# Kernel tuning notes

Hardware: AMD Instinct MI355X
Metric: run time of the kernel (lower is better)

The kernel has to match this reference:

```python
import jax, jax.numpy as jnp
import numpy as np

BITS_MENU = (2, 4, 8)  # fixed candidate bit-widths (replaces torch.unique for jit)
EPS = 1e-8


def _ste_quant_from_stats(x, mn, mx, b):
    # fake-quant with straight-through estimator: identity gradient
    scale = jnp.maximum((mx - mn) / (2.0 ** b - 1.0), EPS)
    q = jnp.round((x - mn) / scale) * scale + mn
    return x + jax.lax.stop_gradient(q - x)


def _ste_quant(x, b):
    return _ste_quant_from_stats(x, x.min(), x.max(), b)


def _conv2d(x, w, b):
    # NCHW / OIHW, stride 1, padding 1 (matches nn.Conv2d(32,32,3,1,1))
    y = jax.lax.conv_general_dilated(
        x, w, window_strides=(1, 1), padding=((1, 1), (1, 1)),
        dimension_numbers=("NCHW", "OIHW", "NCHW"))
    return y + b[None, :, None, None]


def setup_inputs() -> dict:
    key = jax.random.key(0)
    k1, k2, k3, k4 = jax.random.split(key, 4)
    B, Cin, Cout, H, W = 32, 32, 32, 192, 192
    x = jax.random.normal(k1, (B, Cin, H, W), dtype=jnp.float32)
    weight = jax.random.normal(k2, (Cout, Cin, 3, 3), dtype=jnp.float32) * 0.05
    bias = jax.random.normal(k3, (Cout,), dtype=jnp.float32) * 0.01
    # per-sample bit widths drawn from {2,4,8}
    bits = (2 ** jax.random.randint(k4, (B,), 1, 4)).astype(jnp.int32)
    return {"x": x, "weight": weight, "bias": bias, "bits": bits}


def reference(x, weight, bias, bits):
    out = jnp.zeros((x.shape[0], weight.shape[0], x.shape[2], x.shape[3]),
                    dtype=x.dtype)
    for b in BITS_MENU:
        mask = bits == b                                # [B]
        has = jnp.any(mask)
        m4 = mask[:, None, None, None]
        # group min/max over the selected samples (matches x[idx].min()/max())
        mn = jnp.min(jnp.where(m4, x, jnp.inf))
        mx = jnp.max(jnp.where(m4, x, -jnp.inf))
        mn = jnp.where(has, mn, 0.0)
        mx = jnp.where(has, mx, 0.0)
        x_q = _ste_quant_from_stats(x, mn, mx, float(b))
        w_q = _ste_quant(weight, float(b))
        y = _conv2d(x_q, w_q, bias)
        out = jnp.where(m4, y, out)  # scatter back to original sample order
    return out
```

## Files before the change

### kernel.cpp

```cpp
#include <hip/hip_runtime.h>

#define EPSQ 1e-8f

typedef int v4i  __attribute__((ext_vector_type(4)));
typedef int v16i __attribute__((ext_vector_type(16)));


__device__ __forceinline__ int bytesum4(int v) {
#if __has_builtin(__builtin_amdgcn_sdot4)
    return __builtin_amdgcn_sdot4(v, 0x01010101, 0, false);
#else
    return (int)(char)(v) + (int)(char)(v >> 8) + (int)(char)(v >> 16) + (int)(char)(v >> 24);
#endif
}

__global__ __launch_bounds__(256) void kAW(
    const float* __restrict__ x, const float* __restrict__ w,
    float* __restrict__ partials, unsigned int* __restrict__ wq8,
    int* __restrict__ colJ, float* __restrict__ wstats)
{
    __shared__ float smn[256], smx[256];
    __shared__ int   jred[256];
    __shared__ float s_wmn, s_wmx;
    const int tid = threadIdx.x;

    if (blockIdx.x < 1152) {
        const int batch = blockIdx.x / 36;
        const int blk   = blockIdx.x % 36;
        const float* xb = x + (size_t)batch * 1179648 + (size_t)blk * 32768;
        float mn = INFINITY, mx = -INFINITY;
#pragma unroll
        for (int i = 0; i < 32; ++i) {
            const float4 v = reinterpret_cast<const float4*>(xb)[i * 256 + tid];
            mn = fminf(mn, fminf(fminf(v.x, v.y), fminf(v.z, v.w)));
            mx = fmaxf(mx, fmaxf(fmaxf(v.x, v.y), fmaxf(v.z, v.w)));
        }
        smn[tid] = mn; smx[tid] = mx;
        __syncthreads();
        for (int s = 128; s > 0; s >>= 1) {
            if (tid < s) {
                smn[tid] = fminf(smn[tid], smn[tid + s]);
                smx[tid] = fmaxf(smx[tid], smx[tid + s]);
            }
            __syncthreads();
        }
        if (tid == 0) {
            partials[blockIdx.x * 2 + 0] = smn[0];
            partials[blockIdx.x * 2 + 1] = smx[0];
        }
        return;
    }

    const int wb  = blockIdx.x - 1152;
    const int g   = wb / 9;
    const int tap = wb % 9;

    float wmn = INFINITY, wmx = -INFINITY;
    for (int i = tid; i < 9216; i += 256) {
        const float v = w[i];
        wmn = fminf(wmn, v); wmx = fmaxf(wmx, v);
    }
    smn[tid] = wmn; smx[tid] = wmx; __syncthreads();
    for (int s = 128; s > 0; s >>= 1) {
        if (tid < s) {
            smn[tid] = fminf(smn[tid], smn[tid + s]);
            smx[tid] = fmaxf(smx[tid], smx[tid + s]);
        }
        __syncthreads();
    }
    if (tid == 0) { s_wmn = smn[0]; s_wmx = smx[0]; }
    __syncthreads();
    if (wb == 0 && tid == 0) { wstats[0] = s_wmn; wstats[1] = s_wmx; }

    const float wmv = s_wmn, wxv = s_wmx;
    const int bval = 2 << g;
    const float denom = (float)((1 << bval) - 1);
    const float t = fmaxf((wxv - wmv) / denom, EPSQ);
    const int sig = 1 << (bval - 1);

    const int co = tid & 31;
    const int q  = tid >> 5;
    unsigned int packed = 0;
    int jsum = 0;
#pragma unroll
    for (int b = 0; b < 4; ++b) {
        const int ci = q * 4 + b;
        int jc = (int)rintf((w[co * 288 + ci * 9 + tap] - wmv) / t) - sig;
        jc = jc < -128 ? -128 : (jc > 127 ? 127 : jc);
        jsum += jc;
        packed |= ((unsigned int)(unsigned char)(char)jc) << (8 * b);
    }
    const int lane_ = (q >> 2) * 32 + co;
    const int a4    = q & 3;
    wq8[((size_t)(g * 9 + tap) * 64 + lane_) * 4 + a4] = packed;

    jred[tid] = jsum; __syncthreads();
    if (tid < 128) jred[tid] += jred[tid + 128];
    __syncthreads();
    if (tid < 64) jred[tid] += jred[tid + 64];
    __syncthreads();
    if (tid < 32) colJ[g * 288 + tap * 32 + tid] = jred[tid] + jred[tid + 32];
}

__global__ __launch_bounds__(256) void kQ_quant(
    const float* __restrict__ x, const int* __restrict__ bits,
    const float* __restrict__ partials, unsigned int* __restrict__ codes)
{
    __shared__ float bmn[32], bmx[32];
    __shared__ float s_mn, s_sc;

    const int n     = blockIdx.x / 36;
    const int chunk = blockIdx.x % 36;
    const int tid   = threadIdx.x;
    const int bval  = bits[n];
    const int sig   = 1 << (bval - 1);

    if (tid < 32) {
        float mn = INFINITY, mx = -INFINITY;
        for (int i = 0; i < 36; ++i) {
            mn = fminf(mn, partials[(tid * 36 + i) * 2 + 0]);
            mx = fmaxf(mx, partials[(tid * 36 + i) * 2 + 1]);
        }
        bmn[tid] = mn; bmx[tid] = mx;
    }
    __syncthreads();
    if (tid == 0) {
        float mn = INFINITY, mx = -INFINITY;
        for (int nb = 0; nb < 32; ++nb)
            if (bits[nb] == bval) { mn = fminf(mn, bmn[nb]); mx = fmaxf(mx, bmx[nb]); }
        const float denom = (float)((1 << bval) - 1);
        s_mn = mn;
        s_sc = fmaxf((mx - mn) / denom, EPSQ);
    }
    __syncthreads();
    const float mn = s_mn, s = s_sc;

    const int px0 = chunk * 1024 + tid * 4;
    const float* xn = x + (size_t)n * 1179648;

    unsigned int creg[32];
#pragma unroll
    for (int i = 0; i < 32; ++i) creg[i] = 0;

#pragma unroll
    for (int ci = 0; ci < 32; ++ci) {
        const float4 v = *(const float4*)(xn + (size_t)ci * 36864 + px0);
        const float vv[4] = {v.x, v.y, v.z, v.w};
#pragma unroll
        for (int p = 0; p < 4; ++p) {
            int kq = (int)rintf((vv[p] - mn) / s) - sig;
            kq = kq < -128 ? -128 : (kq > 127 ? 127 : kq);
            creg[p * 8 + (ci >> 2)] |= ((unsigned int)(unsigned char)(char)kq) << (8 * (ci & 3));
        }
    }

    unsigned int* cp = codes + ((size_t)n * 36864 + (size_t)px0) * 8;
#pragma unroll
    for (int p = 0; p < 4; ++p) {
        *(v4i*)(cp + p * 8 + 0) = (v4i){(int)creg[p*8+0], (int)creg[p*8+1], (int)creg[p*8+2], (int)creg[p*8+3]};
        *(v4i*)(cp + p * 8 + 4) = (v4i){(int)creg[p*8+4], (int)creg[p*8+5], (int)creg[p*8+6], (int)creg[p*8+7]};
    }
}

__global__ __launch_bounds__(256, 4) void kC_codes(
    const unsigned int* __restrict__ codes, const int* __restrict__ bits,
    const float* __restrict__ partials, const int* __restrict__ colJ,
    const float* __restrict__ wstats, const float* __restrict__ bias,
    const unsigned int* __restrict__ wq8, float* __restrict__ out)
{
    __shared__ v4i   xkv[18 * 34 * 3];
    __shared__ short cs2s[18 * 34];
    __shared__ float tlds[288];
    __shared__ float bmn[32], bmx[32];
    __shared__ float s_stats[4];

    const int n  = blockIdx.z;
    const int oy = blockIdx.y * 16;
    const int ox = blockIdx.x * 32;
    const int tid  = threadIdx.x;
    const int lane = tid & 63;
    const int wv   = tid >> 6;

    const int bval = bits[n];
    const int g = (bval == 2) ? 0 : (bval == 4 ? 1 : 2);
    const int sig = 1 << (bval - 1);
    const float denom = (float)((1 << bval) - 1);

    if (tid < 32) {
        float mn = INFINITY, mx = -INFINITY;
        for (int i = 0; i < 36; ++i) {
            mn = fminf(mn, partials[(tid * 36 + i) * 2 + 0]);
            mx = fmaxf(mx, partials[(tid * 36 + i) * 2 + 1]);
        }
        bmn[tid] = mn; bmx[tid] = mx;
    }
    __syncthreads();
    if (tid == 0) {
        float mn = INFINITY, mx = -INFINITY;
        for (int nb = 0; nb < 32; ++nb)
            if (bits[nb] == bval) { mn = fminf(mn, bmn[nb]); mx = fmaxf(mx, bmx[nb]); }
        const float scale = fmaxf((mx - mn) / denom, EPSQ);
        const float wmv = wstats[0], wxv = wstats[1];
        const float t = fmaxf((wxv - wmv) / denom, EPSQ);
        const double B_ = (double)wmv + (double)sig * (double)t;
        s_stats[0] = mn;
        s_stats[1] = scale;
        s_stats[2] = (float)((double)scale * (double)t);
        s_stats[3] = (float)((double)scale * B_);
    }
    __syncthreads();
    const float C1 = s_stats[2];
    const float C2 = s_stats[3];

    {
        const float wmv = wstats[0], wxv = wstats[1];
        const float t = fmaxf((wxv - wmv) / denom, EPSQ);
        const double A_ = (double)s_stats[0] + (double)sig * (double)s_stats[1];
        const double B_ = (double)wmv + (double)sig * (double)t;
        for (int idx = tid; idx < 288; idx += 256) {
            const int cls = idx / 32;
            const int co  = idx % 32;
            const int rc = cls / 3, cc = cls % 3;
            double js = 0.0, ij = 0.0; int ninv = 0;
            for (int tap = 0; tap < 9; ++tap) {
                const int dy = tap / 3, dx = tap % 3;
                const int cj = colJ[g * 288 + tap * 32 + co];
                js += (double)cj;
                const bool inv = (rc == 0 && dy == 0) || (rc == 2 && dy == 2) ||
                                 (cc == 0 && dx == 0) || (cc == 2 && dx == 2);
                if (inv) { ++ninv; ij += (double)cj; }
            }
            const double v = (double)t * A_ * js + 288.0 * A_ * B_ + (double)bias[co]
                           - A_ * (32.0 * B_ * (double)ninv + (double)t * ij);
            tlds[idx] = (float)v;
        }
    }

    const v4i* wA = (const v4i*)(wq8 + (size_t)g * 2304);
    v4i wfr[9];
#pragma unroll
    for (int t = 0; t < 9; ++t) wfr[t] = wA[t * 64 + lane];

    const unsigned int* cb = codes + (size_t)n * 36864 * 8;
    char* xk = (char*)xkv;
    for (int px = tid; px < 612; px += 256) {
        const int r = px / 34;
        const int c = px - r * 34;
        const int gy = oy + r - 1, gx = ox + c - 1;
        v4i pk0 = (v4i){0,0,0,0}, pk1 = (v4i){0,0,0,0};
        int ksum = 0;
        if (((unsigned)gy < 192u) && ((unsigned)gx < 192u)) {
            const unsigned int* p = cb + ((size_t)gy * 192 + gx) * 8;
            pk0 = *(const v4i*)(p + 0);
            pk1 = *(const v4i*)(p + 4);
            ksum = bytesum4(pk0.x) + bytesum4(pk0.y) + bytesum4(pk0.z) + bytesum4(pk0.w)
                 + bytesum4(pk1.x) + bytesum4(pk1.y) + bytesum4(pk1.z) + bytesum4(pk1.w);
        }
        *(v4i*)(xk + px * 48 +  0) = pk0;
        *(v4i*)(xk + px * 48 + 16) = pk1;
        cs2s[px] = (short)ksum;
    }
    __syncthreads();

    const int c  = lane & 31;
    const int ch = lane >> 5;
    const int gx = ox + c;
    const int cc = (gx == 0) ? 0 : ((gx == 191) ? 2 : 1);
    const int r0 = wv * 4;

    v16i acc[4] = {};
#pragma unroll
    for (int dyr = 0; dyr < 6; ++dyr) {
        const int xrow = r0 + dyr;
        const v4i bf0 = xkv[(xrow * 34 + c + 0) * 3 + ch];
        const v4i bf1 = xkv[(xrow * 34 + c + 1) * 3 + ch];
        const v4i bf2 = xkv[(xrow * 34 + c + 2) * 3 + ch];
#pragma unroll
        for (int m = 0; m < 4; ++m) {
            const int dy = dyr - m;
            if (dy >= 0 && dy < 3) {
                acc[m] = __builtin_amdgcn_mfma_i32_32x32x32_i8(wfr[dy * 3 + 0], bf0, acc[m], 0, 0, 0);
                acc[m] = __builtin_amdgcn_mfma_i32_32x32x32_i8(wfr[dy * 3 + 1], bf1, acc[m], 0, 0, 0);
                acc[m] = __builtin_amdgcn_mfma_i32_32x32x32_i8(wfr[dy * 3 + 2], bf2, acc[m], 0, 0, 0);
            }
        }
    }

#pragma unroll
    for (int m = 0; m < 4; ++m) {
        const int r  = r0 + m;
        const int gy = oy + r;
        int k1 = 0;
#pragma unroll
        for (int dy = 0; dy < 3; ++dy)
#pragma unroll
            for (int dx = 0; dx < 3; ++dx)
                k1 += (int)cs2s[(r + dy) * 34 + (c + dx)];
        const int rc = (gy == 0) ? 0 : ((gy == 191) ? 2 : 1);
        const int cls = rc * 3 + cc;
        const float t2 = C2 * (float)k1;
#pragma unroll
        for (int reg = 0; reg < 16; ++reg) {
            const int co = (reg & 3) + 8 * (reg >> 2) + 4 * ch;
            const float y = fmaf(C1, (float)acc[m][reg], t2 + tlds[cls * 32 + co]);
            out[(((size_t)n * 32 + co) * 192 + gy) * 192 + gx] = y;
        }
    }
}

__global__ __launch_bounds__(256) void kB2_stats_tbl(
    const float* __restrict__ bias, const int* __restrict__ bits,
    const float* __restrict__ partials, const int* __restrict__ colJ,
    const float* __restrict__ wstats,
    float* __restrict__ gstats, float* __restrict__ coefs, float* __restrict__ tbl)
{
    __shared__ float bmn[32], bmx[32];
    __shared__ float s_gmn[3], s_gs[3];
    const int tid = threadIdx.x;
    const float wmv = wstats[0], wxv = wstats[1];

    if (tid < 32) {
        float mn = INFINITY, mx = -INFINITY;
        for (int i = 0; i < 36; ++i) {
            mn = fminf(mn, partials[(tid * 36 + i) * 2 + 0]);
            mx = fmaxf(mx, partials[(tid * 36 + i) * 2 + 1]);
        }
        bmn[tid] = mn; bmx[tid] = mx;
    }
    __syncthreads();

    if (tid < 3) {
        const int bval = 2 << tid;
        const float denom = (float)((1 << bval) - 1);
        float mn = INFINITY, mx = -INFINITY; bool has = false;
        for (int nb = 0; nb < 32; ++nb) {
            if (bits[nb] == bval) { has = true; mn = fminf(mn, bmn[nb]); mx = fmaxf(mx, bmx[nb]); }
        }
        if (!has) { mn = 0.f; mx = 0.f; }
        const float scale = fmaxf((mx - mn) / denom, EPSQ);
        gstats[tid * 2 + 0] = mn;
        gstats[tid * 2 + 1] = scale;
        s_gmn[tid] = mn; s_gs[tid] = scale;

        const float t = fmaxf((wxv - wmv) / denom, EPSQ);
        const int sig = 1 << (bval - 1);
        const double B_ = (double)wmv + (double)sig * (double)t;
        coefs[tid * 2 + 0] = (float)((double)scale * (double)t);
        coefs[tid * 2 + 1] = (float)((double)scale * B_);
    }
    __syncthreads();

    for (int idx = tid; idx < 864; idx += 256) {
        const int g   = idx / 288;
        const int rem = idx % 288;
        const int cls = rem / 32;
        const int co  = rem % 32;
        const int bval = 2 << g;
        const float denom = (float)((1 << bval) - 1);
        const float t = fmaxf((wxv - wmv) / denom, EPSQ);
        const int sig = 1 << (bval - 1);
        const double A_ = (double)s_gmn[g] + (double)sig * (double)s_gs[g];
        const double B_ = (double)wmv + (double)sig * (double)t;
        const int rc = cls / 3, cc = cls % 3;
        double js = 0.0, ij = 0.0; int ninv = 0;
        for (int tap = 0; tap < 9; ++tap) {
            const int dy = tap / 3, dx = tap % 3;
            const int cj = colJ[g * 288 + tap * 32 + co];
            js += (double)cj;
            const bool inv = (rc == 0 && dy == 0) || (rc == 2 && dy == 2) ||
                             (cc == 0 && dx == 0) || (cc == 2 && dx == 2);
            if (inv) { ++ninv; ij += (double)cj; }
        }
        const double v = (double)t * A_ * js + 288.0 * A_ * B_ + (double)bias[co]
                       - A_ * (32.0 * B_ * (double)ninv + (double)t * ij);
        tbl[idx] = (float)v;
    }
}

__global__ __launch_bounds__(256, 4) void kC_fused(
    const float* __restrict__ x, const int* __restrict__ bits,
    const float* __restrict__ gstats, const float* __restrict__ coefs,
    const float* __restrict__ tbl, const unsigned int* __restrict__ wq8,
    float* __restrict__ out)
{
    __shared__ v4i   xkv[18 * 34 * 3];
    __shared__ short cs2s[18 * 34];
    __shared__ float tlds[288];

    const int n  = blockIdx.z;
    const int oy = blockIdx.y * 16;
    const int ox = blockIdx.x * 32;
    const int tid  = threadIdx.x;
    const int lane = tid & 63;
    const int wv   = tid >> 6;

    const int bval = bits[n];
    const int g = (bval == 2) ? 0 : (bval == 4 ? 1 : 2);
    const int sig = 1 << (bval - 1);
    const float mn = gstats[g * 2 + 0];
    const float s  = gstats[g * 2 + 1];
    const float C1 = coefs[g * 2 + 0];
    const float C2 = coefs[g * 2 + 1];

    const v4i* wA = (const v4i*)(wq8 + (size_t)g * 2304);
    v4i wfr[9];
#pragma unroll
    for (int t = 0; t < 9; ++t) wfr[t] = wA[t * 64 + lane];

    for (int i = tid; i < 288; i += 256) tlds[i] = tbl[g * 288 + i];

    const float* xn = x + (size_t)n * 1179648;
    char* xk = (char*)xkv;
    for (int px = tid; px < 612; px += 256) {
        const int r = px / 34;
        const int c = px - r * 34;
        const int gy = oy + r - 1, gx = ox + c - 1;
        const bool valid = ((unsigned)gy < 192u) && ((unsigned)gx < 192u);
        const float* xp = xn + (size_t)(valid ? gy : 0) * 192 + (valid ? gx : 0);
        int ksum = 0;
        v4i pk0, pk1;
#pragma unroll
        for (int h = 0; h < 2; ++h) {
            float v[16];
#pragma unroll
            for (int i = 0; i < 16; ++i) v[i] = xp[(size_t)(h * 16 + i) * 36864];
            int w4[4];
#pragma unroll
            for (int q4 = 0; q4 < 4; ++q4) {
                unsigned int pw = 0;
#pragma unroll
                for (int b = 0; b < 4; ++b) {
                    int kq = (int)rintf((v[q4 * 4 + b] - mn) / s) - sig;
                    kq = kq < -128 ? -128 : (kq > 127 ? 127 : kq);
                    ksum += kq;
                    pw |= ((unsigned int)(unsigned char)(char)kq) << (8 * b);
                }
                w4[q4] = (int)pw;
            }
            if (h == 0) pk0 = (v4i){w4[0], w4[1], w4[2], w4[3]};
            else        pk1 = (v4i){w4[0], w4[1], w4[2], w4[3]};
        }
        if (!valid) { pk0 = (v4i){0,0,0,0}; pk1 = (v4i){0,0,0,0}; ksum = 0; }
        *(v4i*)(xk + px * 48 +  0) = pk0;
        *(v4i*)(xk + px * 48 + 16) = pk1;
        cs2s[px] = (short)ksum;
    }
    __syncthreads();

    const int c  = lane & 31;
    const int ch = lane >> 5;
    const int gx = ox + c;
    const int cc = (gx == 0) ? 0 : ((gx == 191) ? 2 : 1);
    const int r0 = wv * 4;

    v16i acc[4] = {};
#pragma unroll
    for (int dyr = 0; dyr < 6; ++dyr) {
        const int xrow = r0 + dyr;
        const v4i bf0 = xkv[(xrow * 34 + c + 0) * 3 + ch];
        const v4i bf1 = xkv[(xrow * 34 + c + 1) * 3 + ch];
        const v4i bf2 = xkv[(xrow * 34 + c + 2) * 3 + ch];
#pragma unroll
        for (int m = 0; m < 4; ++m) {
            const int dy = dyr - m;
            if (dy >= 0 && dy < 3) {
                acc[m] = __builtin_amdgcn_mfma_i32_32x32x32_i8(wfr[dy * 3 + 0], bf0, acc[m], 0, 0, 0);
                acc[m] = __builtin_amdgcn_mfma_i32_32x32x32_i8(wfr[dy * 3 + 1], bf1, acc[m], 0, 0, 0);
                acc[m] = __builtin_amdgcn_mfma_i32_32x32x32_i8(wfr[dy * 3 + 2], bf2, acc[m], 0, 0, 0);
            }
        }
    }

#pragma unroll
    for (int m = 0; m < 4; ++m) {
        const int r  = r0 + m;
        const int gy = oy + r;
        int k1 = 0;
#pragma unroll
        for (int dy = 0; dy < 3; ++dy)
#pragma unroll
            for (int dx = 0; dx < 3; ++dx)
                k1 += (int)cs2s[(r + dy) * 34 + (c + dx)];
        const int rc = (gy == 0) ? 0 : ((gy == 191) ? 2 : 1);
        const int cls = rc * 3 + cc;
        const float t2 = C2 * (float)k1;
#pragma unroll
        for (int reg = 0; reg < 16; ++reg) {
            const int co = (reg & 3) + 8 * (reg >> 2) + 4 * ch;
            const float y = fmaf(C1, (float)acc[m][reg], t2 + tlds[cls * 32 + co]);
            out[(((size_t)n * 32 + co) * 192 + gy) * 192 + gx] = y;
        }
    }
}

extern "C" void kernel_launch(void* const* d_in, const int* in_sizes, int n_in,
                              void* d_out, int out_size, void* d_ws, size_t ws_size,
                              hipStream_t stream) {
    const float* x      = (const float*)d_in[0];
    const float* weight = (const float*)d_in[1];
    const float* bias   = (const float*)d_in[2];
    const int*   bits   = (const int*)d_in[3];
    float* out = (float*)d_out;

    float* ws       = (float*)d_ws;
    float* partials = ws;
    float* gstats   = ws + 2304;
    float* coefs    = ws + 2312;
    float* tbl      = ws + 2320;
    int*   colJ     = (int*)(ws + 3184);
    unsigned int* wq8 = (unsigned int*)(ws + 4048);
    float* wstats   = ws + 10960;
    const size_t codes_off   = 43904;
    const size_t codes_bytes = 37748736ull;
    unsigned int* codes = (unsigned int*)((char*)d_ws + codes_off);
    const bool big_ws = ws_size >= codes_off + codes_bytes;

    kAW<<<1179, 256, 0, stream>>>(x, weight, partials, wq8, colJ, wstats);

    dim3 grid(6, 12, 32);
    if (big_ws) {
        kQ_quant<<<32 * 36, 256, 0, stream>>>(x, bits, partials, codes);
        kC_codes<<<grid, 256, 0, stream>>>(codes, bits, partials, colJ, wstats, bias, wq8, out);
    } else {
        kB2_stats_tbl<<<1, 256, 0, stream>>>(bias, bits, partials, colJ, wstats, gstats, coefs, tbl);
        kC_fused<<<grid, 256, 0, stream>>>(x, bits, gstats, coefs, tbl, wq8, out);
    }
}
```

Measured before the change: 118.6 us.

## Fuse stats, quantize and conv phases into one cooperative persistent kernel

Merges the min/max reduction, activation quantization and int8 conv into a single cooperative kernel with grid-wide syncs between phases, removing two kernel launch boundaries. The work units are also split more finely (72 chunks per sample instead of 36) for better load balance across the 777 persistent blocks. If a cooperative launch is unavailable, it falls back to three separate kernels. The cost is grid-sync overhead, forced persistent scheduling with limited occupancy, and extra per-block host-side occupancy queries on every call.

```diff
diff --git a/kernel.cpp b/kernel.cpp
--- a/kernel.cpp
+++ b/kernel.cpp
@@ -1,4 +1,7 @@
 #include <hip/hip_runtime.h>
+#include <hip/hip_cooperative_groups.h>
+
+namespace cg = cooperative_groups;
 
 #define EPSQ 1e-8f
 
@@ -14,24 +17,24 @@
 #endif
 }
 
-__global__ __launch_bounds__(256) void kAW(
-    const float* __restrict__ x, const float* __restrict__ w,
+__device__ __forceinline__ void phaseA_unit(
+    int u, int tid, const float* __restrict__ x, const float* __restrict__ w,
     float* __restrict__ partials, unsigned int* __restrict__ wq8,
-    int* __restrict__ colJ, float* __restrict__ wstats)
-{
-    __shared__ float smn[256], smx[256];
-    __shared__ int   jred[256];
-    __shared__ float s_wmn, s_wmx;
-    const int tid = threadIdx.x;
-
-    if (blockIdx.x < 1152) {
-        const int batch = blockIdx.x / 36;
-        const int blk   = blockIdx.x % 36;
-        const float* xb = x + (size_t)batch * 1179648 + (size_t)blk * 32768;
+    int* __restrict__ colJ, float* __restrict__ wstats, char* smem)
+{
+    float* smn  = (float*)smem;
+    float* smx  = (float*)(smem + 1024);
+    int*   jred = (int*)(smem + 2048);
+    float* swst = (float*)(smem + 3072);
+
+    if (u < 2304) {
+        const int batch = u / 72;
+        const int blk   = u % 72;
+        const float4* xb4 = (const float4*)(x + (size_t)batch * 1179648 + (size_t)blk * 16384);
         float mn = INFINITY, mx = -INFINITY;
 #pragma unroll
-        for (int i = 0; i < 32; ++i) {
-            const float4 v = reinterpret_cast<const float4*>(xb)[i * 256 + tid];
+        for (int i = 0; i < 16; ++i) {
+            const float4 v = xb4[i * 256 + tid];
             mn = fminf(mn, fminf(fminf(v.x, v.y), fminf(v.z, v.w)));
             mx = fmaxf(mx, fmaxf(fmaxf(v.x, v.y), fmaxf(v.z, v.w)));
         }
@@ -45,13 +48,14 @@
             __syncthreads();
         }
         if (tid == 0) {
-            partials[blockIdx.x * 2 + 0] = smn[0];
-            partials[blockIdx.x * 2 + 1] = smx[0];
-        }
+            partials[u * 2 + 0] = smn[0];
+            partials[u * 2 + 1] = smx[0];
+        }
+        __syncthreads();
         return;
     }
 
-    const int wb  = blockIdx.x - 1152;
+    const int wb  = u - 2304;
     const int g   = wb / 9;
     const int tap = wb % 9;
 
@@ -68,11 +72,11 @@
         }
         __syncthreads();
     }
-    if (tid == 0) { s_wmn = smn[0]; s_wmx = smx[0]; }
-    __syncthreads();
-    if (wb == 0 && tid == 0) { wstats[0] = s_wmn; wstats[1] = s_wmx; }
-
-    const float wmv = s_wmn, wxv = s_wmx;
+    if (tid == 0) { swst[0] = smn[0]; swst[1] = smx[0]; }
+    __syncthreads();
+    if (wb == 0 && tid == 0) { wstats[0] = swst[0]; wstats[1] = swst[1]; }
+
+    const float wmv = swst[0], wxv = swst[1];
     const int bval = 2 << g;
     const float denom = (float)((1 << bval) - 1);
     const float t = fmaxf((wxv - wmv) / denom, EPSQ);
@@ -100,26 +104,27 @@
     if (tid < 64) jred[tid] += jred[tid + 64];
     __syncthreads();
     if (tid < 32) colJ[g * 288 + tap * 32 + tid] = jred[tid] + jred[tid + 32];
-}
-
-__global__ __launch_bounds__(256) void kQ_quant(
-    const float* __restrict__ x, const int* __restrict__ bits,
-    const float* __restrict__ partials, unsigned int* __restrict__ codes)
-{
-    __shared__ float bmn[32], bmx[32];
-    __shared__ float s_mn, s_sc;
-
-    const int n     = blockIdx.x / 36;
-    const int chunk = blockIdx.x % 36;
-    const int tid   = threadIdx.x;
+    __syncthreads();
+}
+
+__device__ __forceinline__ void phaseQ_unit(
+    int u, int tid, const float* __restrict__ x, const int* __restrict__ bits,
+    const float* __restrict__ partials, unsigned int* __restrict__ codes, char* smem)
+{
+    float* bmn = (float*)smem;
+    float* bmx = (float*)(smem + 128);
+    float* s2  = (float*)(smem + 256);
+
+    const int n     = u / 72;
+    const int chunk = u % 72;
     const int bval  = bits[n];
     const int sig   = 1 << (bval - 1);
 
     if (tid < 32) {
         float mn = INFINITY, mx = -INFINITY;
-        for (int i = 0; i < 36; ++i) {
-            mn = fminf(mn, partials[(tid * 36 + i) * 2 + 0]);
-            mx = fmaxf(mx, partials[(tid * 36 + i) * 2 + 1]);
+        for (int i = 0; i < 72; ++i) {
+            mn = fminf(mn, partials[(tid * 72 + i) * 2 + 0]);
+            mx = fmaxf(mx, partials[(tid * 72 + i) * 2 + 1]);
         }
         bmn[tid] = mn; bmx[tid] = mx;
     }
@@ -129,25 +134,25 @@
         for (int nb = 0; nb < 32; ++nb)
             if (bits[nb] == bval) { mn = fminf(mn, bmn[nb]); mx = fmaxf(mx, bmx[nb]); }
         const float denom = (float)((1 << bval) - 1);
-        s_mn = mn;
-        s_sc = fmaxf((mx - mn) / denom, EPSQ);
-    }
-    __syncthreads();
-    const float mn = s_mn, s = s_sc;
-
-    const int px0 = chunk * 1024 + tid * 4;
+        s2[0] = mn;
+        s2[1] = fmaxf((mx - mn) / denom, EPSQ);
+    }
+    __syncthreads();
+    const float mn = s2[0], s = s2[1];
+
+    const int px0 = chunk * 512 + tid * 2;
     const float* xn = x + (size_t)n * 1179648;
 
-    unsigned int creg[32];
-#pragma unroll
-    for (int i = 0; i < 32; ++i) creg[i] = 0;
+    unsigned int creg[16];
+#pragma unroll
+    for (int i = 0; i < 16; ++i) creg[i] = 0;
 
 #pragma unroll
     for (int ci = 0; ci < 32; ++ci) {
-        const float4 v = *(const float4*)(xn + (size_t)ci * 36864 + px0);
-        const float vv[4] = {v.x, v.y, v.z, v.w};
-#pragma unroll
-        for (int p = 0; p < 4; ++p) {
+        const float2 v = *(const float2*)(xn + (size_t)ci * 36864 + px0);
+        const float vv[2] = {v.x, v.y};
+#pragma unroll
+        for (int p = 0; p < 2; ++p) {
             int kq = (int)rintf((vv[p] - mn) / s) - sig;
             kq = kq < -128 ? -128 : (kq > 127 ? 127 : kq);
             creg[p * 8 + (ci >> 2)] |= ((unsigned int)(unsigned char)(char)kq) << (8 * (ci & 3));
@@ -156,28 +161,31 @@
 
     unsigned int* cp = codes + ((size_t)n * 36864 + (size_t)px0) * 8;
 #pragma unroll
-    for (int p = 0; p < 4; ++p) {
+    for (int p = 0; p < 2; ++p) {
         *(v4i*)(cp + p * 8 + 0) = (v4i){(int)creg[p*8+0], (int)creg[p*8+1], (int)creg[p*8+2], (int)creg[p*8+3]};
         *(v4i*)(cp + p * 8 + 4) = (v4i){(int)creg[p*8+4], (int)creg[p*8+5], (int)creg[p*8+6], (int)creg[p*8+7]};
     }
-}
-
-__global__ __launch_bounds__(256, 4) void kC_codes(
-    const unsigned int* __restrict__ codes, const int* __restrict__ bits,
+    __syncthreads();
+}
+
+__device__ __forceinline__ void phaseC_tile(
+    int t, int tid, const unsigned int* __restrict__ codes, const int* __restrict__ bits,
     const float* __restrict__ partials, const int* __restrict__ colJ,
     const float* __restrict__ wstats, const float* __restrict__ bias,
-    const unsigned int* __restrict__ wq8, float* __restrict__ out)
-{
-    __shared__ v4i   xkv[18 * 34 * 3];
-    __shared__ short cs2s[18 * 34];
-    __shared__ float tlds[288];
-    __shared__ float bmn[32], bmx[32];
-    __shared__ float s_stats[4];
-
-    const int n  = blockIdx.z;
-    const int oy = blockIdx.y * 16;
-    const int ox = blockIdx.x * 32;
-    const int tid  = threadIdx.x;
+    const unsigned int* __restrict__ wq8, float* __restrict__ out, char* smem)
+{
+    v4i*   xkv  = (v4i*)smem;
+    short* cs2s = (short*)(smem + 29376);
+    float* tlds = (float*)(smem + 30600);
+    float* bmn  = (float*)(smem + 31752);
+    float* bmx  = (float*)(smem + 31880);
+    float* sst  = (float*)(smem + 32008);
+
+    const int bx = t % 6;
+    const int by = (t / 6) % 12;
+    const int n  = t / 72;
+    const int oy = by * 16;
+    const int ox = bx * 32;
     const int lane = tid & 63;
     const int wv   = tid >> 6;
 
@@ -188,9 +196,9 @@
 
     if (tid < 32) {
         float mn = INFINITY, mx = -INFINITY;
-        for (int i = 0; i < 36; ++i) {
-            mn = fminf(mn, partials[(tid * 36 + i) * 2 + 0]);
-            mx = fmaxf(mx, partials[(tid * 36 + i) * 2 + 1]);
+        for (int i = 0; i < 72; ++i) {
+            mn = fminf(mn, partials[(tid * 72 + i) * 2 + 0]);
+            mx = fmaxf(mx, partials[(tid * 72 + i) * 2 + 1]);
         }
         bmn[tid] = mn; bmx[tid] = mx;
     }
@@ -201,22 +209,22 @@
             if (bits[nb] == bval) { mn = fminf(mn, bmn[nb]); mx = fmaxf(mx, bmx[nb]); }
         const float scale = fmaxf((mx - mn) / denom, EPSQ);
         const float wmv = wstats[0], wxv = wstats[1];
-        const float t = fmaxf((wxv - wmv) / denom, EPSQ);
-        const double B_ = (double)wmv + (double)sig * (double)t;
-        s_stats[0] = mn;
-        s_stats[1] = scale;
-        s_stats[2] = (float)((double)scale * (double)t);
-        s_stats[3] = (float)((double)scale * B_);
-    }
-    __syncthreads();
-    const float C1 = s_stats[2];
-    const float C2 = s_stats[3];
+        const float tq = fmaxf((wxv - wmv) / denom, EPSQ);
+        const double B_ = (double)wmv + (double)sig * (double)tq;
+        sst[0] = mn;
+        sst[1] = scale;
+        sst[2] = (float)((double)scale * (double)tq);
+        sst[3] = (float)((double)scale * B_);
+    }
+    __syncthreads();
+    const float C1 = sst[2];
+    const float C2 = sst[3];
 
     {
         const float wmv = wstats[0], wxv = wstats[1];
-        const float t = fmaxf((wxv - wmv) / denom, EPSQ);
-        const double A_ = (double)s_stats[0] + (double)sig * (double)s_stats[1];
-        const double B_ = (double)wmv + (double)sig * (double)t;
+        const float tq = fmaxf((wxv - wmv) / denom, EPSQ);
+        const double A_ = (double)sst[0] + (double)sig * (double)sst[1];
+        const double B_ = (double)wmv + (double)sig * (double)tq;
         for (int idx = tid; idx < 288; idx += 256) {
             const int cls = idx / 32;
             const int co  = idx % 32;
@@ -230,8 +238,8 @@
                                  (cc == 0 && dx == 0) || (cc == 2 && dx == 2);
                 if (inv) { ++ninv; ij += (double)cj; }
             }
-            const double v = (double)t * A_ * js + 288.0 * A_ * B_ + (double)bias[co]
-                           - A_ * (32.0 * B_ * (double)ninv + (double)t * ij);
+            const double v = (double)tq * A_ * js + 288.0 * A_ * B_ + (double)bias[co]
+                           - A_ * (32.0 * B_ * (double)ninv + (double)tq * ij);
             tlds[idx] = (float)v;
         }
     }
@@ -239,7 +247,7 @@
     const v4i* wA = (const v4i*)(wq8 + (size_t)g * 2304);
     v4i wfr[9];
 #pragma unroll
-    for (int t = 0; t < 9; ++t) wfr[t] = wA[t * 64 + lane];
+    for (int tt = 0; tt < 9; ++tt) wfr[tt] = wA[tt * 64 + lane];
 
     const unsigned int* cb = codes + (size_t)n * 36864 * 8;
     char* xk = (char*)xkv;
@@ -306,6 +314,146 @@
             out[(((size_t)n * 32 + co) * 192 + gy) * 192 + gx] = y;
         }
     }
+}
+
+__global__ __launch_bounds__(256, 4) void kMega(
+    const float* __restrict__ x, const float* __restrict__ w,
+    const float* __restrict__ bias, const int* __restrict__ bits,
+    float* __restrict__ partials, unsigned int* __restrict__ wq8,
+    int* __restrict__ colJ, float* __restrict__ wstats,
+    unsigned int* __restrict__ codes, float* __restrict__ out)
+{
+    __shared__ __align__(16) char smem[32032];
+    const int tid = threadIdx.x;
+    cg::grid_group grid = cg::this_grid();
+
+    for (int u = blockIdx.x; u < 2331; u += gridDim.x)
+        phaseA_unit(u, tid, x, w, partials, wq8, colJ, wstats, smem);
+    __threadfence();
+    grid.sync();
+
+    for (int u = blockIdx.x; u < 2304; u += gridDim.x)
+        phaseQ_unit(u, tid, x, bits, partials, codes, smem);
+    __threadfence();
+    grid.sync();
+
+    for (int t = blockIdx.x; t < 2304; t += gridDim.x)
+        phaseC_tile(t, tid, codes, bits, partials, colJ, wstats, bias, wq8, out, smem);
+}
+
+__global__ __launch_bounds__(256) void kPhaseA(
+    const float* __restrict__ x, const float* __restrict__ w,
+    float* __restrict__ partials, unsigned int* __restrict__ wq8,
+    int* __restrict__ colJ, float* __restrict__ wstats)
+{
+    __shared__ __align__(16) char smem[3080];
+    if (blockIdx.x < 2331) phaseA_unit(blockIdx.x, threadIdx.x, x, w, partials, wq8, colJ, wstats, smem);
+}
+
+__global__ __launch_bounds__(256) void kPhaseQ(
+    const float* __restrict__ x, const int* __restrict__ bits,
+    const float* __restrict__ partials, unsigned int* __restrict__ codes)
+{
+    __shared__ __align__(16) char smem[264];
+    if (blockIdx.x < 2304) phaseQ_unit(blockIdx.x, threadIdx.x, x, bits, partials, codes, smem);
+}
+
+__global__ __launch_bounds__(256, 4) void kPhaseC(
+    const unsigned int* __restrict__ codes, const int* __restrict__ bits,
+    const float* __restrict__ partials, const int* __restrict__ colJ,
+    const float* __restrict__ wstats, const float* __restrict__ bias,
+    const unsigned int* __restrict__ wq8, float* __restrict__ out)
+{
+    __shared__ __align__(16) char smem[32032];
+    if (blockIdx.x < 2304) phaseC_tile(blockIdx.x, threadIdx.x, codes, bits, partials, colJ, wstats, bias, wq8, out, smem);
+}
+
+__global__ __launch_bounds__(256) void kAW_legacy(
+    const float* __restrict__ x, const float* __restrict__ w,
+    float* __restrict__ partials, unsigned int* __restrict__ wq8,
+    int* __restrict__ colJ, float* __restrict__ wstats)
+{
+    __shared__ float smn[256], smx[256];
+    __shared__ int   jred[256];
+    __shared__ float s_wmn, s_wmx;
+    const int tid = threadIdx.x;
+
+    if (blockIdx.x < 1152) {
+        const int batch = blockIdx.x / 36;
+        const int blk   = blockIdx.x % 36;
+        const float* xb = x + (size_t)batch * 1179648 + (size_t)blk * 32768;
+        float mn = INFINITY, mx = -INFINITY;
+#pragma unroll
+        for (int i = 0; i < 32; ++i) {
+            const float4 v = reinterpret_cast<const float4*>(xb)[i * 256 + tid];
+            mn = fminf(mn, fminf(fminf(v.x, v.y), fminf(v.z, v.w)));
+            mx = fmaxf(mx, fmaxf(fmaxf(v.x, v.y), fmaxf(v.z, v.w)));
+        }
+        smn[tid] = mn; smx[tid] = mx;
+        __syncthreads();
+        for (int s = 128; s > 0; s >>= 1) {
+            if (tid < s) {
+                smn[tid] = fminf(smn[tid], smn[tid + s]);
+                smx[tid] = fmaxf(smx[tid], smx[tid + s]);
+            }
+            __syncthreads();
+        }
+        if (tid == 0) {
+            partials[blockIdx.x * 2 + 0] = smn[0];
+            partials[blockIdx.x * 2 + 1] = smx[0];
+        }
+        return;
+    }
+
+    const int wb  = blockIdx.x - 1152;
+    const int g   = wb / 9;
+    const int tap = wb % 9;
+
+    float wmn = INFINITY, wmx = -INFINITY;
+    for (int i = tid; i < 9216; i += 256) {
+        const float v = w[i];
+        wmn = fminf(wmn, v); wmx = fmaxf(wmx, v);
+    }
+    smn[tid] = wmn; smx[tid] = wmx; __syncthreads();
+    for (int s = 128; s > 0; s >>= 1) {
+        if (tid < s) {
+            smn[tid] = fminf(smn[tid], smn[tid + s]);
+            smx[tid] = fmaxf(smx[tid], smx[tid + s]);
+        }
+        __syncthreads();
+    }
+    if (tid == 0) { s_wmn = smn[0]; s_wmx = smx[0]; }
+    __syncthreads();
+    if (wb == 0 && tid == 0) { wstats[0] = s_wmn; wstats[1] = s_wmx; }
+
+    const float wmv = s_wmn, wxv = s_wmx;
+    const int bval = 2 << g;
+    const float denom = (float)((1 << bval) - 1);
+    const float t = fmaxf((wxv - wmv) / denom, EPSQ);
+    const int sig = 1 << (bval - 1);
+
+    const int co = tid & 31;
+    const int q  = tid >> 5;
+    unsigned int packed = 0;
+    int jsum = 0;
+#pragma unroll
+    for (int b = 0; b < 4; ++b) {
+        const int ci = q * 4 + b;
+        int jc = (int)rintf((w[co * 288 + ci * 9 + tap] - wmv) / t) - sig;
+        jc = jc < -128 ? -128 : (jc > 127 ? 127 : jc);
+        jsum += jc;
+        packed |= ((unsigned int)(unsigned char)(char)jc) << (8 * b);
+    }
+    const int lane_ = (q >> 2) * 32 + co;
+    const int a4    = q & 3;
+    wq8[((size_t)(g * 9 + tap) * 64 + lane_) * 4 + a4] = packed;
+
+    jred[tid] = jsum; __syncthreads();
+    if (tid < 128) jred[tid] += jred[tid + 128];
+    __syncthreads();
+    if (tid < 64) jred[tid] += jred[tid + 64];
+    __syncthreads();
+    if (tid < 32) colJ[g * 288 + tap * 32 + tid] = jred[tid] + jred[tid + 32];
 }
 
 __global__ __launch_bounds__(256) void kB2_stats_tbl(
@@ -502,27 +650,45 @@
     const int*   bits   = (const int*)d_in[3];
     float* out = (float*)d_out;
 
-    float* ws       = (float*)d_ws;
+    float* ws = (float*)d_ws;
     float* partials = ws;
-    float* gstats   = ws + 2304;
-    float* coefs    = ws + 2312;
-    float* tbl      = ws + 2320;
-    int*   colJ     = (int*)(ws + 3184);
-    unsigned int* wq8 = (unsigned int*)(ws + 4048);
-    float* wstats   = ws + 10960;
-    const size_t codes_off   = 43904;
+    int*   colJ     = (int*)(ws + 4608);
+    unsigned int* wq8 = (unsigned int*)(ws + 5472);
+    float* wstats   = ws + 12384;
+    float* lpart    = ws + 12416;
+    float* gstats   = ws + 14720;
+    float* coefs    = ws + 14728;
+    float* tbl      = ws + 14736;
+    const size_t codes_off   = 62464;
     const size_t codes_bytes = 37748736ull;
     unsigned int* codes = (unsigned int*)((char*)d_ws + codes_off);
     const bool big_ws = ws_size >= codes_off + codes_bytes;
 
-    kAW<<<1179, 256, 0, stream>>>(x, weight, partials, wq8, colJ, wstats);
-
+    if (big_ws) {
+        const int coopGrid = 777;
+        int maxPerCU = 0;
+        hipError_t qe = hipOccupancyMaxActiveBlocksPerMultiprocessor(&maxPerCU, kMega, 256, 0);
+        int coopAttr = 0;
+        int dev = 0;
+        hipGetDevice(&dev);
+        hipDeviceGetAttribute(&coopAttr, hipDeviceAttributeCooperativeLaunch, dev);
+
+        if (qe == hipSuccess && coopAttr && (size_t)maxPerCU * 256 >= (size_t)coopGrid) {
+            void* args[] = {(void*)&x, (void*)&weight, (void*)&bias, (void*)&bits,
+                            (void*)&partials, (void*)&wq8, (void*)&colJ, (void*)&wstats,
+                            (void*)&codes, (void*)&out};
+            hipError_t le = hipLaunchCooperativeKernel(kMega, dim3(coopGrid), dim3(256),
+                                                       args, 0, stream);
+            if (le == hipSuccess) return;
+        }
+        kPhaseA<<<2331, 256, 0, stream>>>(x, weight, partials, wq8, colJ, wstats);
+        kPhaseQ<<<2304, 256, 0, stream>>>(x, bits, partials, codes);
+        kPhaseC<<<2304, 256, 0, stream>>>(codes, bits, partials, colJ, wstats, bias, wq8, out);
+        return;
+    }
+
+    kAW_legacy<<<1179, 256, 0, stream>>>(x, weight, lpart, wq8, colJ, wstats);
+    kB2_stats_tbl<<<1, 256, 0, stream>>>(bias, bits, lpart, colJ, wstats, gstats, coefs, tbl);
     dim3 grid(6, 12, 32);
-    if (big_ws) {
-        kQ_quant<<<32 * 36, 256, 0, stream>>>(x, bits, partials, codes);
-        kC_codes<<<grid, 256, 0, stream>>>(codes, bits, partials, colJ, wstats, bias, wq8, out);
-    } else {
-        kB2_stats_tbl<<<1, 256, 0, stream>>>(bias, bits, partials, colJ, wstats, gstats, coefs, tbl);
-        kC_fused<<<grid, 256, 0, stream>>>(x, bits, gstats, coefs, tbl, wq8, out);
-    }
-}
+    kC_fused<<<grid, 256, 0, stream>>>(x, bits, gstats, coefs, tbl, wq8, out);
+}
```

After: 134.0 us. +12.9%, slower.

## Hoist per-group stats and bias table into quant kernel; reuse row sums

Applied to the files above, without the earlier changes.

Block 0 of the quantization kernel now computes the per-group scale coefficients and the 864-entry bias/correction table once. The conv kernel no longer has each of its 2304 blocks re-reduce the min/max partials and rebuild a 288-entry double-precision table; it just loads the precomputed values. The epilogue's 3x3 code-sum is restructured to reuse per-row horizontal sums across the four output rows, and output stores become nontemporal. The cost is extra serial work in block 0 of the quant kernel, plus a small extra global read in the conv kernel.

```diff
diff --git a/kernel.cpp b/kernel.cpp
--- a/kernel.cpp
+++ b/kernel.cpp
@@ -104,10 +104,14 @@
 
 __global__ __launch_bounds__(256) void kQ_quant(
     const float* __restrict__ x, const int* __restrict__ bits,
-    const float* __restrict__ partials, unsigned int* __restrict__ codes)
+    const float* __restrict__ partials, const int* __restrict__ colJ,
+    const float* __restrict__ wstats, const float* __restrict__ bias,
+    unsigned int* __restrict__ codes,
+    float* __restrict__ coefs, float* __restrict__ tbl)
 {
     __shared__ float bmn[32], bmx[32];
     __shared__ float s_mn, s_sc;
+    __shared__ float s_gmn[3], s_gs[3];
 
     const int n     = blockIdx.x / 36;
     const int chunk = blockIdx.x % 36;
@@ -135,91 +139,37 @@
     __syncthreads();
     const float mn = s_mn, s = s_sc;
 
-    const int px0 = chunk * 1024 + tid * 4;
-    const float* xn = x + (size_t)n * 1179648;
-
-    unsigned int creg[32];
-#pragma unroll
-    for (int i = 0; i < 32; ++i) creg[i] = 0;
-
-#pragma unroll
-    for (int ci = 0; ci < 32; ++ci) {
-        const float4 v = *(const float4*)(xn + (size_t)ci * 36864 + px0);
-        const float vv[4] = {v.x, v.y, v.z, v.w};
-#pragma unroll
-        for (int p = 0; p < 4; ++p) {
-            int kq = (int)rintf((vv[p] - mn) / s) - sig;
-            kq = kq < -128 ? -128 : (kq > 127 ? 127 : kq);
-            creg[p * 8 + (ci >> 2)] |= ((unsigned int)(unsigned char)(char)kq) << (8 * (ci & 3));
-        }
-    }
-
-    unsigned int* cp = codes + ((size_t)n * 36864 + (size_t)px0) * 8;
-#pragma unroll
-    for (int p = 0; p < 4; ++p) {
-        *(v4i*)(cp + p * 8 + 0) = (v4i){(int)creg[p*8+0], (int)creg[p*8+1], (int)creg[p*8+2], (int)creg[p*8+3]};
-        *(v4i*)(cp + p * 8 + 4) = (v4i){(int)creg[p*8+4], (int)creg[p*8+5], (int)creg[p*8+6], (int)creg[p*8+7]};
-    }
-}
-
-__global__ __launch_bounds__(256, 4) void kC_codes(
-    const unsigned int* __restrict__ codes, const int* __restrict__ bits,
-    const float* __restrict__ partials, const int* __restrict__ colJ,
-    const float* __restrict__ wstats, const float* __restrict__ bias,
-    const unsigned int* __restrict__ wq8, float* __restrict__ out)
-{
-    __shared__ v4i   xkv[18 * 34 * 3];
-    __shared__ short cs2s[18 * 34];
-    __shared__ float tlds[288];
-    __shared__ float bmn[32], bmx[32];
-    __shared__ float s_stats[4];
-
-    const int n  = blockIdx.z;
-    const int oy = blockIdx.y * 16;
-    const int ox = blockIdx.x * 32;
-    const int tid  = threadIdx.x;
-    const int lane = tid & 63;
-    const int wv   = tid >> 6;
-
-    const int bval = bits[n];
-    const int g = (bval == 2) ? 0 : (bval == 4 ? 1 : 2);
-    const int sig = 1 << (bval - 1);
-    const float denom = (float)((1 << bval) - 1);
-
-    if (tid < 32) {
-        float mn = INFINITY, mx = -INFINITY;
-        for (int i = 0; i < 36; ++i) {
-            mn = fminf(mn, partials[(tid * 36 + i) * 2 + 0]);
-            mx = fmaxf(mx, partials[(tid * 36 + i) * 2 + 1]);
-        }
-        bmn[tid] = mn; bmx[tid] = mx;
-    }
-    __syncthreads();
-    if (tid == 0) {
-        float mn = INFINITY, mx = -INFINITY;
-        for (int nb = 0; nb < 32; ++nb)
-            if (bits[nb] == bval) { mn = fminf(mn, bmn[nb]); mx = fmaxf(mx, bmx[nb]); }
-        const float scale = fmaxf((mx - mn) / denom, EPSQ);
+    if (blockIdx.x == 0) {
         const float wmv = wstats[0], wxv = wstats[1];
-        const float t = fmaxf((wxv - wmv) / denom, EPSQ);
-        const double B_ = (double)wmv + (double)sig * (double)t;
-        s_stats[0] = mn;
-        s_stats[1] = scale;
-        s_stats[2] = (float)((double)scale * (double)t);
-        s_stats[3] = (float)((double)scale * B_);
-    }
-    __syncthreads();
-    const float C1 = s_stats[2];
-    const float C2 = s_stats[3];
-
-    {
-        const float wmv = wstats[0], wxv = wstats[1];
-        const float t = fmaxf((wxv - wmv) / denom, EPSQ);
-        const double A_ = (double)s_stats[0] + (double)sig * (double)s_stats[1];
-        const double B_ = (double)wmv + (double)sig * (double)t;
-        for (int idx = tid; idx < 288; idx += 256) {
-            const int cls = idx / 32;
-            const int co  = idx % 32;
+        if (tid < 3) {
+            const int bv = 2 << tid;
+            const float denom = (float)((1 << bv) - 1);
+            float gmn = INFINITY, gmx = -INFINITY; bool has = false;
+            for (int nb = 0; nb < 32; ++nb) {
+                if (bits[nb] == bv) { has = true; gmn = fminf(gmn, bmn[nb]); gmx = fmaxf(gmx, bmx[nb]); }
+            }
+            if (!has) { gmn = 0.f; gmx = 0.f; }
+            const float scale = fmaxf((gmx - gmn) / denom, EPSQ);
+            s_gmn[tid] = gmn; s_gs[tid] = scale;
+
+            const float t = fmaxf((wxv - wmv) / denom, EPSQ);
+            const int sg = 1 << (bv - 1);
+            const double B_ = (double)wmv + (double)sg * (double)t;
+            coefs[tid * 2 + 0] = (float)((double)scale * (double)t);
+            coefs[tid * 2 + 1] = (float)((double)scale * B_);
+        }
+        __syncthreads();
+        for (int idx = tid; idx < 864; idx += 256) {
+            const int g   = idx / 288;
+            const int rem = idx % 288;
+            const int cls = rem / 32;
+            const int co  = rem % 32;
+            const int bv = 2 << g;
+            const float denom = (float)((1 << bv) - 1);
+            const float t = fmaxf((wxv - wmv) / denom, EPSQ);
+            const int sg = 1 << (bv - 1);
+            const double A_ = (double)s_gmn[g] + (double)sg * (double)s_gs[g];
+            const double B_ = (double)wmv + (double)sg * (double)t;
             const int rc = cls / 3, cc = cls % 3;
             double js = 0.0, ij = 0.0; int ninv = 0;
             for (int tap = 0; tap < 9; ++tap) {
@@ -232,14 +182,64 @@
             }
             const double v = (double)t * A_ * js + 288.0 * A_ * B_ + (double)bias[co]
                            - A_ * (32.0 * B_ * (double)ninv + (double)t * ij);
-            tlds[idx] = (float)v;
-        }
-    }
+            tbl[idx] = (float)v;
+        }
+    }
+
+    const int px0 = chunk * 1024 + tid * 4;
+    const float* xn = x + (size_t)n * 1179648;
+
+    unsigned int creg[32];
+#pragma unroll
+    for (int i = 0; i < 32; ++i) creg[i] = 0;
+
+#pragma unroll
+    for (int ci = 0; ci < 32; ++ci) {
+        const float4 v = *(const float4*)(xn + (size_t)ci * 36864 + px0);
+        const float vv[4] = {v.x, v.y, v.z, v.w};
+#pragma unroll
+        for (int p = 0; p < 4; ++p) {
+            int kq = (int)rintf((vv[p] - mn) / s) - sig;
+            kq = kq < -128 ? -128 : (kq > 127 ? 127 : kq);
+            creg[p * 8 + (ci >> 2)] |= ((unsigned int)(unsigned char)(char)kq) << (8 * (ci & 3));
+        }
+    }
+
+    unsigned int* cp = codes + ((size_t)n * 36864 + (size_t)px0) * 8;
+#pragma unroll
+    for (int p = 0; p < 4; ++p) {
+        *(v4i*)(cp + p * 8 + 0) = (v4i){(int)creg[p*8+0], (int)creg[p*8+1], (int)creg[p*8+2], (int)creg[p*8+3]};
+        *(v4i*)(cp + p * 8 + 4) = (v4i){(int)creg[p*8+4], (int)creg[p*8+5], (int)creg[p*8+6], (int)creg[p*8+7]};
+    }
+}
+
+__global__ __launch_bounds__(256, 4) void kC_codes(
+    const unsigned int* __restrict__ codes, const int* __restrict__ bits,
+    const float* __restrict__ coefs, const float* __restrict__ tbl,
+    const unsigned int* __restrict__ wq8, float* __restrict__ out)
+{
+    __shared__ v4i   xkv[18 * 34 * 3];
+    __shared__ short cs2s[18 * 34];
+    __shared__ float tlds[288];
+
+    const int n  = blockIdx.z;
+    const int oy = blockIdx.y * 16;
+    const int ox = blockIdx.x * 32;
+    const int tid  = threadIdx.x;
+    const int lane = tid & 63;
+    const int wv   = tid >> 6;
+
+    const int bval = bits[n];
+    const int g = (bval == 2) ? 0 : (bval == 4 ? 1 : 2);
+    const float C1 = coefs[g * 2 + 0];
+    const float C2 = coefs[g * 2 + 1];
 
     const v4i* wA = (const v4i*)(wq8 + (size_t)g * 2304);
     v4i wfr[9];
 #pragma unroll
     for (int t = 0; t < 9; ++t) wfr[t] = wA[t * 64 + lane];
+
+    for (int i = tid; i < 288; i += 256) tlds[i] = tbl[g * 288 + i];
 
     const unsigned int* cb = codes + (size_t)n * 36864 * 8;
     char* xk = (char*)xkv;
@@ -286,16 +286,17 @@
         }
     }
 
+    int rs[6];
+#pragma unroll
+    for (int dy = 0; dy < 6; ++dy) {
+        const int row = r0 + dy;
+        rs[dy] = (int)cs2s[row * 34 + c] + (int)cs2s[row * 34 + c + 1] + (int)cs2s[row * 34 + c + 2];
+    }
+
 #pragma unroll
     for (int m = 0; m < 4; ++m) {
-        const int r  = r0 + m;
-        const int gy = oy + r;
-        int k1 = 0;
-#pragma unroll
-        for (int dy = 0; dy < 3; ++dy)
-#pragma unroll
-            for (int dx = 0; dx < 3; ++dx)
-                k1 += (int)cs2s[(r + dy) * 34 + (c + dx)];
+        const int gy = oy + r0 + m;
+        const int k1 = rs[m] + rs[m + 1] + rs[m + 2];
         const int rc = (gy == 0) ? 0 : ((gy == 191) ? 2 : 1);
         const int cls = rc * 3 + cc;
         const float t2 = C2 * (float)k1;
@@ -303,7 +304,7 @@
         for (int reg = 0; reg < 16; ++reg) {
             const int co = (reg & 3) + 8 * (reg >> 2) + 4 * ch;
             const float y = fmaf(C1, (float)acc[m][reg], t2 + tlds[cls * 32 + co]);
-            out[(((size_t)n * 32 + co) * 192 + gy) * 192 + gx] = y;
+            __builtin_nontemporal_store(y, &out[(((size_t)n * 32 + co) * 192 + gy) * 192 + gx]);
         }
     }
 }
@@ -519,8 +520,8 @@
 
     dim3 grid(6, 12, 32);
     if (big_ws) {
-        kQ_quant<<<32 * 36, 256, 0, stream>>>(x, bits, partials, codes);
-        kC_codes<<<grid, 256, 0, stream>>>(codes, bits, partials, colJ, wstats, bias, wq8, out);
+        kQ_quant<<<32 * 36, 256, 0, stream>>>(x, bits, partials, colJ, wstats, bias, codes, coefs, tbl);
+        kC_codes<<<grid, 256, 0, stream>>>(codes, bits, coefs, tbl, wq8, out);
     } else {
         kB2_stats_tbl<<<1, 256, 0, stream>>>(bias, bits, partials, colJ, wstats, gstats, coefs, tbl);
         kC_fused<<<grid, 256, 0, stream>>>(x, bits, gstats, coefs, tbl, wq8, out);
```

Result: faster. 110.4 us (-7.0%).
